# Optimization experiments

Hardware: AMD Instinct MI355X
Metric: run time of the kernel (lower is better)

The kernel has to match this reference:

```python
import jax, jax.numpy as jnp
import numpy as np

P = 2048
IMG_H = IMG_W = 128
FOV = 1.0471975512  # 60 deg vertical/horizontal fov
ZNEAR, ZFAR = 0.01, 100.0
SH_C0 = 0.28209479177387814
LOWPASS = 0.3  # 3DGS low-pass filter added to 2D covariance diagonal


def _camera():
    view = np.eye(4, dtype=np.float32)
    view[2, 3] = 4.0  # camera at world z=-4 looking down +z
    tanf = np.tan(FOV / 2)
    pm = np.zeros((4, 4), dtype=np.float32)
    pm[0, 0] = 1.0 / tanf
    pm[1, 1] = 1.0 / tanf
    pm[2, 2] = ZFAR / (ZFAR - ZNEAR)
    pm[2, 3] = -ZFAR * ZNEAR / (ZFAR - ZNEAR)
    pm[3, 2] = 1.0
    proj = (pm @ view).astype(np.float32)
    campos = np.array([0.0, 0.0, -4.0], dtype=np.float32)
    return view, proj, campos


def setup_inputs() -> dict:
    key = jax.random.key(0)
    ks = jax.random.split(key, 6)
    view, proj, campos = _camera()
    return {
        'means_3d': jax.random.normal(ks[0], (P, 3), dtype=jnp.float32) * 0.8,
        'means_2d': jnp.zeros((P, 2), dtype=jnp.float32),
        'features': jax.random.uniform(ks[1], (P, 3), dtype=jnp.float32),
        'opacities': jax.random.uniform(ks[2], (P, 1), dtype=jnp.float32) * 0.9 + 0.05,
        'scales': jax.random.uniform(ks[3], (P, 3), dtype=jnp.float32) * 0.08 + 0.01,
        'rotations': jax.random.normal(ks[4], (P, 4), dtype=jnp.float32),
        'viewmatrix': jnp.asarray(view),
        'projmatrix': jnp.asarray(proj),
        'campos': jnp.asarray(campos),
        'image_height': IMG_H,
        'image_width': IMG_W,
    }


def _quat_to_rot(q):
    q = q / jnp.linalg.norm(q, axis=-1, keepdims=True)
    w, x, y, z = q[:, 0], q[:, 1], q[:, 2], q[:, 3]
    R = jnp.stack([
        1 - 2 * (y * y + z * z), 2 * (x * y - w * z), 2 * (x * z + w * y),
        2 * (x * y + w * z), 1 - 2 * (x * x + z * z), 2 * (y * z - w * x),
        2 * (x * z - w * y), 2 * (y * z + w * x), 1 - 2 * (x * x + y * y),
    ], axis=-1).reshape(-1, 3, 3)
    return R


def _rasterize(means_3d, features, opacities, scales, rotations, viewmatrix, projmatrix, H, W):
    tanf = jnp.tan(FOV / 2)
    focal_x = W / (2.0 * tanf)
    focal_y = H / (2.0 * tanf)

    # camera-space positions [P,3]
    t = means_3d @ viewmatrix[:3, :3].T + viewmatrix[:3, 3]
    depth = t[:, 2]

    # projected pixel centers (ndc2pix)
    ph = means_3d @ projmatrix[:3, :3].T + projmatrix[:3, 3]
    pw = means_3d @ projmatrix[3, :3] + projmatrix[3, 3]
    ndc = ph[:, :2] / (pw[:, None] + 1e-7)
    px = ((ndc[:, 0] + 1.0) * W - 1.0) * 0.5
    py = ((ndc[:, 1] + 1.0) * H - 1.0) * 0.5

    # 3D covariance: Sigma = R S S^T R^T
    Rm = _quat_to_rot(rotations)
    M = Rm * scales[:, None, :]  # R @ diag(s)
    sigma = M @ jnp.swapaxes(M, 1, 2)  # [P,3,3]

    # EWA splat: 2D covariance = J W Sigma W^T J^T
    lim = 1.3 * tanf
    tz = depth
    tx = jnp.clip(t[:, 0] / tz, -lim, lim) * tz
    ty = jnp.clip(t[:, 1] / tz, -lim, lim) * tz
    zeros = jnp.zeros_like(tz)
    J = jnp.stack([
        jnp.stack([focal_x / tz, zeros, -focal_x * tx / (tz * tz)], -1),
        jnp.stack([zeros, focal_y / tz, -focal_y * ty / (tz * tz)], -1),
    ], axis=1)  # [P,2,3]
    Tm = J @ viewmatrix[:3, :3]
    cov2d = Tm @ sigma @ jnp.swapaxes(Tm, 1, 2)  # [P,2,2]
    a = cov2d[:, 0, 0] + LOWPASS
    b = cov2d[:, 0, 1]
    c = cov2d[:, 1, 1] + LOWPASS
    det = a * c - b * b
    valid = (depth > 0.2) & (det > 0.0)
    det_s = jnp.where(valid, det, 1.0)
    conic_a, conic_b, conic_c = c / det_s, -b / det_s, a / det_s

    # radii from max eigenvalue
    mid = 0.5 * (a + c)
    lam = mid + jnp.sqrt(jnp.maximum(mid * mid - det, 0.1))
    radii = jnp.where(valid, jnp.ceil(3.0 * jnp.sqrt(lam)), 0.0)

    # SH degree-0 color
    color = jnp.maximum(SH_C0 * features + 0.5, 0.0)  # [P,3]

    # depth sort, front to back
    order = jnp.argsort(jnp.where(valid, depth, jnp.inf))
    px_s, py_s = px[order], py[order]
    ca, cb, cc = conic_a[order], conic_b[order], conic_c[order]
    op_s = opacities[order, 0]
    col_s = color[order]
    valid_s = valid[order]

    # pixel grid
    gx, gy = jnp.meshgrid(jnp.arange(W, dtype=jnp.float32), jnp.arange(H, dtype=jnp.float32))
    gx = gx.reshape(-1)
    gy = gy.reshape(-1)  # [HW]

    dx = gx[None, :] - px_s[:, None]  # [P,HW]
    dy = gy[None, :] - py_s[:, None]
    power = -0.5 * (ca[:, None] * dx * dx + cc[:, None] * dy * dy) - cb[:, None] * dx * dy
    alpha = jnp.minimum(0.99, op_s[:, None] * jnp.exp(jnp.minimum(power, 0.0)))
    skip = (power > 0.0) | (alpha < 1.0 / 255.0) | (~valid_s)[:, None]
    alpha = jnp.where(skip, 0.0, alpha)

    one_m = 1.0 - alpha
    incl = jnp.cumprod(one_m, axis=0)
    T_excl = jnp.concatenate([jnp.ones((1, H * W), dtype=alpha.dtype), incl[:-1]], axis=0)
    w = T_excl * alpha  # [P,HW]
    img = jnp.einsum('pn,pc->cn', w, col_s)  # [3,HW]
    T_final = incl[-1]
    img = img + T_final[None, :]  # bg_color = (1,1,1)
    return img.reshape(3, H, W), radii


def reference(means_3d, means_2d, features, opacities, scales, rotations, viewmatrix, projmatrix, campos, image_height, image_width):
    # means_2d and campos are interface placeholders (means_2d receives grads only
    # inside the CUDA kernel; campos only matters for sh_degree > 0)
    return _rasterize(means_3d, features, opacities, scales, rotations, viewmatrix, projmatrix, image_height, image_width)
```

## Files before the change

### kernel.cpp

```cpp
#include <hip/hip_runtime.h>
#include <math.h>


#define IMG 128
#define NPIX (IMG * IMG)
#define GS 12
#define SORT_N 2048
#define KCH 16
#define CHUNK (SORT_N / KCH)
#define NTILE 64

typedef unsigned long long u64;

__device__ __forceinline__ void sysStore4(float4* p, float4 v)
{
    union { float f[2]; u64 u; } lo, hi;
    lo.f[0] = v.x; lo.f[1] = v.y; hi.f[0] = v.z; hi.f[1] = v.w;
    u64* q = (u64*)p;
    __hip_atomic_store(q,     lo.u, __ATOMIC_RELAXED, __HIP_MEMORY_SCOPE_SYSTEM);
    __hip_atomic_store(q + 1, hi.u, __ATOMIC_RELAXED, __HIP_MEMORY_SCOPE_SYSTEM);
}
__device__ __forceinline__ float4 sysLoad4(const float4* p)
{
    const u64* q = (const u64*)p;
    u64 a = __hip_atomic_load(q,     __ATOMIC_RELAXED, __HIP_MEMORY_SCOPE_SYSTEM);
    u64 b = __hip_atomic_load(q + 1, __ATOMIC_RELAXED, __HIP_MEMORY_SCOPE_SYSTEM);
    union { u64 u; float f[2]; } lo, hi;
    lo.u = a; hi.u = b;
    return make_float4(lo.f[0], lo.f[1], hi.f[0], hi.f[1]);
}

__device__ __forceinline__ void gproj(int i,
                                      const float* __restrict__ means,
                                      const float* __restrict__ rots,
                                      const float* __restrict__ scales,
                                      const float* __restrict__ vm,
                                      const float* __restrict__ pm,
                                      float& depth, bool& valid,
                                      float& px, float& py,
                                      float& ca, float& cb, float& cc,
                                      float& lam)
{
    const float W = (float)IMG, H = (float)IMG;
    const float tanfov = 0.5773502691896258f;
    const float focal_x = W / (2.0f * tanfov);
    const float focal_y = H / (2.0f * tanfov);
    const float lim = 1.3f * tanfov;

    float mx = means[3 * i + 0], my = means[3 * i + 1], mz = means[3 * i + 2];

    float tx = vm[0] * mx + vm[1] * my + vm[2]  * mz + vm[3];
    float ty = vm[4] * mx + vm[5] * my + vm[6]  * mz + vm[7];
    float tz = vm[8] * mx + vm[9] * my + vm[10] * mz + vm[11];
    depth = tz;

    float ph0 = pm[0]  * mx + pm[1]  * my + pm[2]  * mz + pm[3];
    float ph1 = pm[4]  * mx + pm[5]  * my + pm[6]  * mz + pm[7];
    float pw  = pm[12] * mx + pm[13] * my + pm[14] * mz + pm[15];
    float rinv = 1.0f / (pw + 1e-7f);
    px = ((ph0 * rinv + 1.0f) * W - 1.0f) * 0.5f;
    py = ((ph1 * rinv + 1.0f) * H - 1.0f) * 0.5f;

    float qw = rots[4 * i + 0], qx = rots[4 * i + 1], qy = rots[4 * i + 2], qz = rots[4 * i + 3];
    float qn = sqrtf(qw * qw + qx * qx + qy * qy + qz * qz);
    qw /= qn; qx /= qn; qy /= qn; qz /= qn;
    float R00 = 1.0f - 2.0f * (qy * qy + qz * qz), R01 = 2.0f * (qx * qy - qw * qz), R02 = 2.0f * (qx * qz + qw * qy);
    float R10 = 2.0f * (qx * qy + qw * qz), R11 = 1.0f - 2.0f * (qx * qx + qz * qz), R12 = 2.0f * (qy * qz - qw * qx);
    float R20 = 2.0f * (qx * qz - qw * qy), R21 = 2.0f * (qy * qz + qw * qx), R22 = 1.0f - 2.0f * (qx * qx + qy * qy);

    float sx = scales[3 * i + 0], sy = scales[3 * i + 1], sz = scales[3 * i + 2];
    float M00 = R00 * sx, M01 = R01 * sy, M02 = R02 * sz;
    float M10 = R10 * sx, M11 = R11 * sy, M12 = R12 * sz;
    float M20 = R20 * sx, M21 = R21 * sy, M22 = R22 * sz;
    float S00 = M00 * M00 + M01 * M01 + M02 * M02;
    float S01 = M00 * M10 + M01 * M11 + M02 * M12;
    float S02 = M00 * M20 + M01 * M21 + M02 * M22;
    float S11 = M10 * M10 + M11 * M11 + M12 * M12;
    float S12 = M10 * M20 + M11 * M21 + M12 * M22;
    float S22 = M20 * M20 + M21 * M21 + M22 * M22;

    float txc = fminf(fmaxf(tx / tz, -lim), lim) * tz;
    float tyc = fminf(fmaxf(ty / tz, -lim), lim) * tz;
    float J00 = focal_x / tz, J02 = -focal_x * txc / (tz * tz);
    float J11 = focal_y / tz, J12 = -focal_y * tyc / (tz * tz);

    float T00 = J00 * vm[0] + J02 * vm[8];
    float T01 = J00 * vm[1] + J02 * vm[9];
    float T02 = J00 * vm[2] + J02 * vm[10];
    float T10 = J11 * vm[4] + J12 * vm[8];
    float T11 = J11 * vm[5] + J12 * vm[9];
    float T12 = J11 * vm[6] + J12 * vm[10];

    float U00 = T00 * S00 + T01 * S01 + T02 * S02;
    float U01 = T00 * S01 + T01 * S11 + T02 * S12;
    float U02 = T00 * S02 + T01 * S12 + T02 * S22;
    float U10 = T10 * S00 + T11 * S01 + T12 * S02;
    float U11 = T10 * S01 + T11 * S11 + T12 * S12;
    float U12 = T10 * S02 + T11 * S12 + T12 * S22;
    float C00 = U00 * T00 + U01 * T01 + U02 * T02;
    float C01 = U00 * T10 + U01 * T11 + U02 * T12;
    float C11 = U10 * T10 + U11 * T11 + U12 * T12;

    float a = C00 + 0.3f, b = C01, c = C11 + 0.3f;
    float det = a * c - b * b;
    valid = (depth > 0.2f) && (det > 0.0f);
    float det_s = valid ? det : 1.0f;
    ca = c / det_s; cb = -b / det_s; cc = a / det_s;

    float mid = 0.5f * (a + c);
    lam = mid + sqrtf(fmaxf(mid * mid - det, 0.1f));
}

__global__ void __launch_bounds__(512)
gsplat_prep_rank_scatter(const float* __restrict__ means,
                         const float* __restrict__ feats,
                         const float* __restrict__ ops,
                         const float* __restrict__ scales,
                         const float* __restrict__ rots,
                         const float* __restrict__ vm,
                         const float* __restrict__ pm,
                         float* __restrict__ gS,
                         float4* __restrict__ culls,
                         float* __restrict__ radii_out,
                         unsigned int* __restrict__ tickets,
                         int P)
{
    __shared__ unsigned int sk[SORT_N];
    __shared__ int partial[512];
    int tid = threadIdx.x;

    if (blockIdx.x == 0 && tid < NTILE) tickets[tid] = 0u;

    #pragma unroll 2
    for (int j = tid; j < SORT_N; j += 512) {
        unsigned int key = 0xFFFFFFFFu;
        if (j < P) {
            float mx = means[3 * j + 0], my = means[3 * j + 1], mz = means[3 * j + 2];
            float tz = vm[8] * mx + vm[9] * my + vm[10] * mz + vm[11];
            key = (tz > 0.2f) ? __float_as_uint(tz) : 0x7f800000u;
        }
        sk[j] = key;
    }
    __syncthreads();

    int g = tid & 63, s = tid >> 6;
    int i = blockIdx.x * 64 + g;
    bool act = (i < P);
    unsigned int ki = act ? sk[i] : 0u;

    const int SLICE = SORT_N / 8;
    int j0 = s * SLICE;
    const uint4* sk4 = (const uint4*)(sk + j0);
    int r = 0;
    #pragma unroll 4
    for (int q = 0; q < SLICE / 4; ++q) {
        uint4 k = sk4[q];
        int j = j0 + 4 * q;
        r += (k.x < ki) || (k.x == ki && (j + 0) < i);
        r += (k.y < ki) || (k.y == ki && (j + 1) < i);
        r += (k.z < ki) || (k.z == ki && (j + 2) < i);
        r += (k.w < ki) || (k.w == ki && (j + 3) < i);
    }
    partial[tid] = r;
    __syncthreads();

    if (s == 0 && act) {
        int rank = 0;
        #pragma unroll
        for (int k = 0; k < 8; ++k) rank += partial[64 * k + g];

        float depth, px, py, ca, cb, cc, lam; bool valid;
        gproj(i, means, rots, scales, vm, pm, depth, valid, px, py, ca, cb, cc, lam);

        const float SH_C0 = 0.28209479177387814f;
        float colr = fmaxf(SH_C0 * feats[3 * i + 0] + 0.5f, 0.0f);
        float colg = fmaxf(SH_C0 * feats[3 * i + 1] + 0.5f, 0.0f);
        float colb = fmaxf(SH_C0 * feats[3 * i + 2] + 0.5f, 0.0f);

        float opv = ops[i];
        float r2;
        if (valid) {
            r2 = 2.0f * lam * __logf(255.0f * opv) * 1.02f + 0.5f;
        } else {
            px = 0.0f; py = 0.0f; ca = 0.0f; cb = 0.0f; cc = 0.0f;
            opv = 0.0f; r2 = -1.0f;
        }
        radii_out[i] = valid ? ceilf(3.0f * sqrtf(lam)) : 0.0f;

        float4* dst = (float4*)(gS + (size_t)rank * GS);
        dst[0] = make_float4(px, py, ca, cb);
        dst[1] = make_float4(cc, opv, colr, colg);
        dst[2] = make_float4(colb, r2, 0.0f, 0.0f);
        culls[rank] = make_float4(px, py, r2, 0.0f);
    }
}

__global__ void __launch_bounds__(256, 4)
gsplat_raster_fused(const float* __restrict__ gS,
                    const float4* __restrict__ culls,
                    int P, float4* __restrict__ part,
                    unsigned int* __restrict__ tickets,
                    float* __restrict__ img)
{
    int tid = threadIdx.x;
    int lx = tid & 15, ly = tid >> 4;
    int lane = tid & 63;
    int tile = blockIdx.x;
    int kc = blockIdx.y;
    int tilex = tile & 7, tiley = tile >> 3;
    int x = tilex * 16 + lx, y = tiley * 16 + ly;
    float gx = (float)x, gy = (float)y;
    float tx0 = (float)(tilex * 16), tx1 = (float)(tilex * 16 + 15);
    float ty0 = (float)(tiley * 16), ty1 = (float)(tiley * 16 + 15);

    int base = kc * CHUNK;
    int cnt = min(CHUNK, P - base);

    float T = 1.0f, cr = 0.0f, cg = 0.0f, cb = 0.0f;
    const float* Gp = gS + (size_t)base * GS;

    float4 cu0 = culls[base + lane];
    float4 cu1 = culls[base + 64 + lane];

    #pragma unroll
    for (int half = 0; half < 2; ++half) {
        int h = half * 64;
        float4 cu = (half == 0) ? cu0 : cu1;
        bool pred = false;
        if (h + lane < cnt) {
            float ddx = cu.x - fminf(fmaxf(cu.x, tx0), tx1);
            float ddy = cu.y - fminf(fmaxf(cu.y, ty0), ty1);
            pred = (ddx * ddx + ddy * ddy <= cu.z);
        }
        unsigned long long m = __ballot(pred);
        while (m) {
            int b0 = __builtin_ctzll(m); m &= m - 1;
            int n = 1, b1 = b0, b2 = b0, b3 = b0;
            if (m) { b1 = __builtin_ctzll(m); m &= m - 1; n = 2;
                if (m) { b2 = __builtin_ctzll(m); m &= m - 1; n = 3;
                    if (m) { b3 = __builtin_ctzll(m); m &= m - 1; n = 4; } } }

            const float4* R0 = (const float4*)(Gp + (size_t)(h + b0) * GS);
            const float4* R1 = (const float4*)(Gp + (size_t)(h + b1) * GS);
            const float4* R2 = (const float4*)(Gp + (size_t)(h + b2) * GS);
            const float4* R3 = (const float4*)(Gp + (size_t)(h + b3) * GS);
            float4 A0 = R0[0], B0 = R0[1], C0 = R0[2];
            float4 A1 = R1[0], B1 = R1[1], C1 = R1[2];
            float4 A2 = R2[0], B2 = R2[1], C2 = R2[2];
            float4 A3 = R3[0], B3 = R3[1], C3 = R3[2];

            float dx0 = gx - A0.x, dy0 = gy - A0.y;
            float p0 = -0.5f * (A0.z * dx0 * dx0 + B0.x * dy0 * dy0) - A0.w * dx0 * dy0;
            float a0 = fminf(0.99f, B0.y * __expf(fminf(p0, 0.0f)));
            a0 = (p0 > 0.0f) ? 0.0f : a0;
            a0 = (a0 < 0.00392156862745098f) ? 0.0f : a0;

            float dx1 = gx - A1.x, dy1 = gy - A1.y;
            float p1 = -0.5f * (A1.z * dx1 * dx1 + B1.x * dy1 * dy1) - A1.w * dx1 * dy1;
            float a1 = fminf(0.99f, B1.y * __expf(fminf(p1, 0.0f)));
            a1 = (p1 > 0.0f) ? 0.0f : a1;
            a1 = (a1 < 0.00392156862745098f) ? 0.0f : a1;

            float dx2 = gx - A2.x, dy2 = gy - A2.y;
            float p2 = -0.5f * (A2.z * dx2 * dx2 + B2.x * dy2 * dy2) - A2.w * dx2 * dy2;
            float a2 = fminf(0.99f, B2.y * __expf(fminf(p2, 0.0f)));
            a2 = (p2 > 0.0f) ? 0.0f : a2;
            a2 = (a2 < 0.00392156862745098f) ? 0.0f : a2;

            float dx3 = gx - A3.x, dy3 = gy - A3.y;
            float p3 = -0.5f * (A3.z * dx3 * dx3 + B3.x * dy3 * dy3) - A3.w * dx3 * dy3;
            float a3 = fminf(0.99f, B3.y * __expf(fminf(p3, 0.0f)));
            a3 = (p3 > 0.0f) ? 0.0f : a3;
            a3 = (a3 < 0.00392156862745098f) ? 0.0f : a3;

            float w;
            w = T * a0; cr = fmaf(w, B0.z, cr); cg = fmaf(w, B0.w, cg); cb = fmaf(w, C0.x, cb); T *= (1.0f - a0);
            if (n > 1) { w = T * a1; cr = fmaf(w, B1.z, cr); cg = fmaf(w, B1.w, cg); cb = fmaf(w, C1.x, cb); T *= (1.0f - a1); }
            if (n > 2) { w = T * a2; cr = fmaf(w, B2.z, cr); cg = fmaf(w, B2.w, cg); cb = fmaf(w, C2.x, cb); T *= (1.0f - a2); }
            if (n > 3) { w = T * a3; cr = fmaf(w, B3.z, cr); cg = fmaf(w, B3.w, cg); cb = fmaf(w, C3.x, cb); T *= (1.0f - a3); }
        }
    }

    float4* slab = part + ((size_t)tile * KCH) * 256;
    sysStore4(&slab[kc * 256 + tid], make_float4(cr, cg, cb, T));
    asm volatile("s_waitcnt vmcnt(0)" ::: "memory");
    __syncthreads();
    __shared__ unsigned int s_old;
    if (tid == 0)
        s_old = __hip_atomic_fetch_add(&tickets[tile], 1u,
                                       __ATOMIC_RELAXED, __HIP_MEMORY_SCOPE_SYSTEM);
    __syncthreads();

    if (s_old == KCH - 1) {
        float4 v[8];
        float Tt = 1.0f, r = 0.0f, g = 0.0f, b = 0.0f;
        #pragma unroll
        for (int c = 0; c < 8; ++c) v[c] = sysLoad4(&slab[c * 256 + tid]);
        #pragma unroll
        for (int c = 0; c < 8; ++c) {
            r = fmaf(Tt, v[c].x, r);
            g = fmaf(Tt, v[c].y, g);
            b = fmaf(Tt, v[c].z, b);
            Tt *= v[c].w;
        }
        #pragma unroll
        for (int c = 0; c < 8; ++c) v[c] = sysLoad4(&slab[(8 + c) * 256 + tid]);
        #pragma unroll
        for (int c = 0; c < 8; ++c) {
            r = fmaf(Tt, v[c].x, r);
            g = fmaf(Tt, v[c].y, g);
            b = fmaf(Tt, v[c].z, b);
            Tt *= v[c].w;
        }
        int pix = y * IMG + x;
        img[pix]            = r + Tt;
        img[NPIX + pix]     = g + Tt;
        img[2 * NPIX + pix] = b + Tt;
    }
}

extern "C" void kernel_launch(void* const* d_in, const int* in_sizes, int n_in,
                              void* d_out, int out_size, void* d_ws, size_t ws_size,
                              hipStream_t stream)
{
    const float* means  = (const float*)d_in[0];
    const float* feats  = (const float*)d_in[2];
    const float* ops    = (const float*)d_in[3];
    const float* scales = (const float*)d_in[4];
    const float* rots   = (const float*)d_in[5];
    const float* vm     = (const float*)d_in[6];
    const float* pm     = (const float*)d_in[7];

    int P = in_sizes[0] / 3;

    float* img   = (float*)d_out;
    float* radii = (float*)d_out + 3 * NPIX;

    float*        gS      = (float*)d_ws;
    float4*       culls   = (float4*)(gS + (size_t)SORT_N * GS);
    float4*       part    = culls + SORT_N;
    unsigned int* tickets = (unsigned int*)(part + (size_t)NTILE * KCH * 256);

    gsplat_prep_rank_scatter<<<(P + 63) / 64, 512, 0, stream>>>(
        means, feats, ops, scales, rots, vm, pm, gS, culls, radii, tickets, P);

    gsplat_raster_fused<<<dim3(NTILE, KCH), 256, 0, stream>>>(
        gS, culls, P, part, tickets, img);
}
```

Before: 95.02 us.

## Fuse prep/sort and raster kernels into one persistent launch with grid barrier

Merges the projection/rank-sort kernel and the tile raster kernel into one launch. The first 64 blocks to arrive, picked by an atomic counter, do the sort and scatter work, and every block then spin-waits on a global done counter before rasterizing. All counters reset after the last block passes. This is meant to remove the second launch and the gap between kernels, but it relies on all 1024 blocks being co-resident or on the prep blocks being scheduled first, and it switches the gS and culls accesses to system-scope atomic loads and stores.

```diff
diff --git a/kernel.cpp b/kernel.cpp
--- a/kernel.cpp
+++ b/kernel.cpp
@@ -9,8 +9,15 @@
 #define KCH 16
 #define CHUNK (SORT_N / KCH)
 #define NTILE 64
+#define NPREP 64
+#define PER_UNIT (SORT_N / NPREP)
+#define GRID_TOTAL (NTILE * KCH)
 
 typedef unsigned long long u64;
+
+__device__ unsigned int g_unit   = 0;
+__device__ unsigned int g_done   = 0;
+__device__ unsigned int g_passed = 0;
 
 __device__ __forceinline__ void sysStore4(float4* p, float4 v)
 {
@@ -28,6 +35,12 @@
     union { u64 u; float f[2]; } lo, hi;
     lo.u = a; hi.u = b;
     return make_float4(lo.f[0], lo.f[1], hi.f[0], hi.f[1]);
+}
+__device__ __forceinline__ void sysStore2(float* p, float a, float b)
+{
+    union { float f[2]; u64 u; } v;
+    v.f[0] = a; v.f[1] = b;
+    __hip_atomic_store((u64*)p, v.u, __ATOMIC_RELAXED, __HIP_MEMORY_SCOPE_SYSTEM);
 }
 
 __device__ __forceinline__ void gproj(int i,
@@ -111,102 +124,120 @@
     lam = mid + sqrtf(fmaxf(mid * mid - det, 0.1f));
 }
 
-__global__ void __launch_bounds__(512)
-gsplat_prep_rank_scatter(const float* __restrict__ means,
-                         const float* __restrict__ feats,
-                         const float* __restrict__ ops,
-                         const float* __restrict__ scales,
-                         const float* __restrict__ rots,
-                         const float* __restrict__ vm,
-                         const float* __restrict__ pm,
-                         float* __restrict__ gS,
-                         float4* __restrict__ culls,
-                         float* __restrict__ radii_out,
-                         unsigned int* __restrict__ tickets,
-                         int P)
+__global__ void __launch_bounds__(256, 4)
+gsplat_one(const float* __restrict__ means,
+           const float* __restrict__ feats,
+           const float* __restrict__ ops,
+           const float* __restrict__ scales,
+           const float* __restrict__ rots,
+           const float* __restrict__ vm,
+           const float* __restrict__ pm,
+           float* __restrict__ gS,
+           float4* __restrict__ culls,
+           float* __restrict__ radii_out,
+           float4* __restrict__ part,
+           unsigned int* __restrict__ tickets,
+           float* __restrict__ img,
+           int P)
 {
     __shared__ unsigned int sk[SORT_N];
-    __shared__ int partial[512];
+    __shared__ int partial[256];
+    __shared__ unsigned int s_unit, s_old;
     int tid = threadIdx.x;
-
-    if (blockIdx.x == 0 && tid < NTILE) tickets[tid] = 0u;
-
-    #pragma unroll 2
-    for (int j = tid; j < SORT_N; j += 512) {
-        unsigned int key = 0xFFFFFFFFu;
-        if (j < P) {
-            float mx = means[3 * j + 0], my = means[3 * j + 1], mz = means[3 * j + 2];
-            float tz = vm[8] * mx + vm[9] * my + vm[10] * mz + vm[11];
-            key = (tz > 0.2f) ? __float_as_uint(tz) : 0x7f800000u;
-        }
-        sk[j] = key;
-    }
+    int tile = blockIdx.x;
+    int kc   = blockIdx.y;
+
+    if (tid == 0)
+        s_unit = __hip_atomic_fetch_add(&g_unit, 1u,
+                                        __ATOMIC_RELAXED, __HIP_MEMORY_SCOPE_SYSTEM);
     __syncthreads();
-
-    int g = tid & 63, s = tid >> 6;
-    int i = blockIdx.x * 64 + g;
-    bool act = (i < P);
-    unsigned int ki = act ? sk[i] : 0u;
-
-    const int SLICE = SORT_N / 8;
-    int j0 = s * SLICE;
-    const uint4* sk4 = (const uint4*)(sk + j0);
-    int r = 0;
-    #pragma unroll 4
-    for (int q = 0; q < SLICE / 4; ++q) {
-        uint4 k = sk4[q];
-        int j = j0 + 4 * q;
-        r += (k.x < ki) || (k.x == ki && (j + 0) < i);
-        r += (k.y < ki) || (k.y == ki && (j + 1) < i);
-        r += (k.z < ki) || (k.z == ki && (j + 2) < i);
-        r += (k.w < ki) || (k.w == ki && (j + 3) < i);
-    }
-    partial[tid] = r;
+    unsigned int unit = s_unit;
+
+    if (unit < NPREP) {
+        #pragma unroll 2
+        for (int j = tid; j < SORT_N; j += 256) {
+            unsigned int key = 0xFFFFFFFFu;
+            if (j < P) {
+                float mx = means[3 * j + 0], my = means[3 * j + 1], mz = means[3 * j + 2];
+                float tz = vm[8] * mx + vm[9] * my + vm[10] * mz + vm[11];
+                key = (tz > 0.2f) ? __float_as_uint(tz) : 0x7f800000u;
+            }
+            sk[j] = key;
+        }
+        __syncthreads();
+
+        int g = tid & 31, s = tid >> 5;
+        int i = (int)unit * PER_UNIT + g;
+        bool act = (i < P);
+        unsigned int ki = act ? sk[i] : 0u;
+
+        const int SLICE = SORT_N / 8;
+        int j0 = s * SLICE;
+        const uint4* sk4 = (const uint4*)(sk + j0);
+        int r = 0;
+        #pragma unroll 4
+        for (int q = 0; q < SLICE / 4; ++q) {
+            uint4 k = sk4[q];
+            int j = j0 + 4 * q;
+            r += (k.x < ki) || (k.x == ki && (j + 0) < i);
+            r += (k.y < ki) || (k.y == ki && (j + 1) < i);
+            r += (k.z < ki) || (k.z == ki && (j + 2) < i);
+            r += (k.w < ki) || (k.w == ki && (j + 3) < i);
+        }
+        partial[tid] = r;
+        __syncthreads();
+
+        if (s == 0 && act) {
+            int rank = 0;
+            #pragma unroll
+            for (int k = 0; k < 8; ++k) rank += partial[32 * k + g];
+
+            float depth, px, py, ca, cb, cc, lam; bool valid;
+            gproj(i, means, rots, scales, vm, pm, depth, valid, px, py, ca, cb, cc, lam);
+
+            const float SH_C0 = 0.28209479177387814f;
+            float colr = fmaxf(SH_C0 * feats[3 * i + 0] + 0.5f, 0.0f);
+            float colg = fmaxf(SH_C0 * feats[3 * i + 1] + 0.5f, 0.0f);
+            float colb = fmaxf(SH_C0 * feats[3 * i + 2] + 0.5f, 0.0f);
+
+            float opv = ops[i];
+            float r2;
+            if (valid) {
+                r2 = 2.0f * lam * __logf(255.0f * opv) * 1.02f + 0.5f;
+            } else {
+                px = 0.0f; py = 0.0f; ca = 0.0f; cb = 0.0f; cc = 0.0f;
+                opv = 0.0f; r2 = -1.0f;
+            }
+            radii_out[i] = valid ? ceilf(3.0f * sqrtf(lam)) : 0.0f;
+
+            float* dst = gS + (size_t)rank * GS;
+            sysStore2(dst + 0, px, py);
+            sysStore2(dst + 2, ca, cb);
+            sysStore2(dst + 4, cc, opv);
+            sysStore2(dst + 6, colr, colg);
+            sysStore2(dst + 8, colb, r2);
+            sysStore4(&culls[rank], make_float4(px, py, r2, 0.0f));
+        }
+        if (unit == 0 && tid < NTILE)
+            __hip_atomic_store(&tickets[tid], 0u,
+                               __ATOMIC_RELAXED, __HIP_MEMORY_SCOPE_SYSTEM);
+
+        asm volatile("s_waitcnt vmcnt(0)" ::: "memory");
+        __syncthreads();
+        if (tid == 0)
+            __hip_atomic_fetch_add(&g_done, 1u,
+                                   __ATOMIC_RELAXED, __HIP_MEMORY_SCOPE_SYSTEM);
+    }
+
+    if (tid == 0) {
+        while (__hip_atomic_load(&g_done, __ATOMIC_RELAXED,
+                                 __HIP_MEMORY_SCOPE_SYSTEM) < NPREP)
+            __builtin_amdgcn_s_sleep(8);
+    }
     __syncthreads();
 
-    if (s == 0 && act) {
-        int rank = 0;
-        #pragma unroll
-        for (int k = 0; k < 8; ++k) rank += partial[64 * k + g];
-
-        float depth, px, py, ca, cb, cc, lam; bool valid;
-        gproj(i, means, rots, scales, vm, pm, depth, valid, px, py, ca, cb, cc, lam);
-
-        const float SH_C0 = 0.28209479177387814f;
-        float colr = fmaxf(SH_C0 * feats[3 * i + 0] + 0.5f, 0.0f);
-        float colg = fmaxf(SH_C0 * feats[3 * i + 1] + 0.5f, 0.0f);
-        float colb = fmaxf(SH_C0 * feats[3 * i + 2] + 0.5f, 0.0f);
-
-        float opv = ops[i];
-        float r2;
-        if (valid) {
-            r2 = 2.0f * lam * __logf(255.0f * opv) * 1.02f + 0.5f;
-        } else {
-            px = 0.0f; py = 0.0f; ca = 0.0f; cb = 0.0f; cc = 0.0f;
-            opv = 0.0f; r2 = -1.0f;
-        }
-        radii_out[i] = valid ? ceilf(3.0f * sqrtf(lam)) : 0.0f;
-
-        float4* dst = (float4*)(gS + (size_t)rank * GS);
-        dst[0] = make_float4(px, py, ca, cb);
-        dst[1] = make_float4(cc, opv, colr, colg);
-        dst[2] = make_float4(colb, r2, 0.0f, 0.0f);
-        culls[rank] = make_float4(px, py, r2, 0.0f);
-    }
-}
-
-__global__ void __launch_bounds__(256, 4)
-gsplat_raster_fused(const float* __restrict__ gS,
-                    const float4* __restrict__ culls,
-                    int P, float4* __restrict__ part,
-                    unsigned int* __restrict__ tickets,
-                    float* __restrict__ img)
-{
-    int tid = threadIdx.x;
     int lx = tid & 15, ly = tid >> 4;
     int lane = tid & 63;
-    int tile = blockIdx.x;
-    int kc = blockIdx.y;
     int tilex = tile & 7, tiley = tile >> 3;
     int x = tilex * 16 + lx, y = tiley * 16 + ly;
     float gx = (float)x, gy = (float)y;
@@ -219,8 +250,8 @@
     float T = 1.0f, cr = 0.0f, cg = 0.0f, cb = 0.0f;
     const float* Gp = gS + (size_t)base * GS;
 
-    float4 cu0 = culls[base + lane];
-    float4 cu1 = culls[base + 64 + lane];
+    float4 cu0 = sysLoad4(&culls[base + lane]);
+    float4 cu1 = sysLoad4(&culls[base + 64 + lane]);
 
     #pragma unroll
     for (int half = 0; half < 2; ++half) {
@@ -244,10 +275,10 @@
             const float4* R1 = (const float4*)(Gp + (size_t)(h + b1) * GS);
             const float4* R2 = (const float4*)(Gp + (size_t)(h + b2) * GS);
             const float4* R3 = (const float4*)(Gp + (size_t)(h + b3) * GS);
-            float4 A0 = R0[0], B0 = R0[1], C0 = R0[2];
-            float4 A1 = R1[0], B1 = R1[1], C1 = R1[2];
-            float4 A2 = R2[0], B2 = R2[1], C2 = R2[2];
-            float4 A3 = R3[0], B3 = R3[1], C3 = R3[2];
+            float4 A0 = sysLoad4(R0 + 0), B0 = sysLoad4(R0 + 1), C0 = sysLoad4(R0 + 2);
+            float4 A1 = sysLoad4(R1 + 0), B1 = sysLoad4(R1 + 1), C1 = sysLoad4(R1 + 2);
+            float4 A2 = sysLoad4(R2 + 0), B2 = sysLoad4(R2 + 1), C2 = sysLoad4(R2 + 2);
+            float4 A3 = sysLoad4(R3 + 0), B3 = sysLoad4(R3 + 1), C3 = sysLoad4(R3 + 2);
 
             float dx0 = gx - A0.x, dy0 = gy - A0.y;
             float p0 = -0.5f * (A0.z * dx0 * dx0 + B0.x * dy0 * dy0) - A0.w * dx0 * dy0;
@@ -285,7 +316,6 @@
     sysStore4(&slab[kc * 256 + tid], make_float4(cr, cg, cb, T));
     asm volatile("s_waitcnt vmcnt(0)" ::: "memory");
     __syncthreads();
-    __shared__ unsigned int s_old;
     if (tid == 0)
         s_old = __hip_atomic_fetch_add(&tickets[tile], 1u,
                                        __ATOMIC_RELAXED, __HIP_MEMORY_SCOPE_SYSTEM);
@@ -317,6 +347,16 @@
         img[NPIX + pix]     = g + Tt;
         img[2 * NPIX + pix] = b + Tt;
     }
+
+    if (tid == 0) {
+        unsigned int p = __hip_atomic_fetch_add(&g_passed, 1u,
+                                                __ATOMIC_RELAXED, __HIP_MEMORY_SCOPE_SYSTEM);
+        if (p == GRID_TOTAL - 1) {
+            __hip_atomic_store(&g_unit,   0u, __ATOMIC_RELAXED, __HIP_MEMORY_SCOPE_SYSTEM);
+            __hip_atomic_store(&g_done,   0u, __ATOMIC_RELAXED, __HIP_MEMORY_SCOPE_SYSTEM);
+            __hip_atomic_store(&g_passed, 0u, __ATOMIC_RELAXED, __HIP_MEMORY_SCOPE_SYSTEM);
+        }
+    }
 }
 
 extern "C" void kernel_launch(void* const* d_in, const int* in_sizes, int n_in,
@@ -341,9 +381,7 @@
     float4*       part    = culls + SORT_N;
     unsigned int* tickets = (unsigned int*)(part + (size_t)NTILE * KCH * 256);
 
-    gsplat_prep_rank_scatter<<<(P + 63) / 64, 512, 0, stream>>>(
-        means, feats, ops, scales, rots, vm, pm, gS, culls, radii, tickets, P);
-
-    gsplat_raster_fused<<<dim3(NTILE, KCH), 256, 0, stream>>>(
-        gS, culls, P, part, tickets, img);
-}
+    gsplat_one<<<dim3(NTILE, KCH), 256, 0, stream>>>(
+        means, feats, ops, scales, rots, vm, pm,
+        gS, culls, radii, part, tickets, img, P);
+}
```

Measured after the change: 125.3 us. 1.32x slower.
